# Kernel tuning notes

Measured on AMD Instinct MI355X. Metric: run time of the kernel, lower is better.

## Reference

```python
import jax, jax.numpy as jnp
import numpy as np

B, L, D, H = 2, 2048, 1024, 16
HD = D // H
ROPE_BASE = 10000.0


def _chain_info(lengths):
    """lengths: [B, L] int, chain lengths packed at the front, zeros after.
    Returns per-position within-chain positions (RoPE resets per chain),
    chain ids, and a validity mask."""
    def one(row):
        csum = jnp.cumsum(row)                      # [L]
        total = csum[-1]
        p = jnp.arange(L)
        cid = jnp.searchsorted(csum, p, side='right')  # chain id per position
        prev = jnp.where(cid > 0, csum[jnp.clip(cid - 1, 0, L - 1)], 0)
        valid = p < total
        pos = jnp.where(valid, p - prev, 0).astype(jnp.float32)
        return pos, cid, valid
    return jax.vmap(one)(lengths)


def _rope_tables(pos):
    # pos: [B, L] float -> cos/sin [B, L, 1, HD]
    inv_freq = 1.0 / (ROPE_BASE ** (jnp.arange(0, HD, 2, dtype=jnp.float32) / HD))
    freqs = pos[..., None] * inv_freq               # [B, L, HD/2]
    emb = jnp.concatenate([freqs, freqs], axis=-1)  # [B, L, HD]
    return jnp.cos(emb)[:, :, None, :], jnp.sin(emb)[:, :, None, :]


def _apply_rope(x, cos, sin):
    d = x.shape[-1]
    x1, x2 = x[..., : d // 2], x[..., d // 2:]
    return x * cos + jnp.concatenate([-x2, x1], axis=-1) * sin


def _branch(x, Wqkv, bqkv, cos, sin, allowed):
    # x: [B, L, D]; allowed: [B, L, L] bool attention mask for this branch
    qkv = x @ Wqkv.T + bqkv                          # [B, L, 3D]
    qkv = qkv.reshape(B, L, 3, H, HD)
    q, k, v = qkv[:, :, 0], qkv[:, :, 1], qkv[:, :, 2]
    q = q * (HD ** -0.5)
    q = _apply_rope(q, cos, sin)
    k = _apply_rope(k, cos, sin)
    scores = jnp.einsum('bthd,bshd->bhts', q, k)     # [B, H, L, L]
    scores = jnp.where(allowed[:, None], scores, -jnp.inf)
    probs = jax.nn.softmax(scores, axis=-1)
    probs = jnp.where(jnp.isnan(probs), 0.0, probs)  # fully-masked rows -> 0
    out = jnp.einsum('bhts,bshd->bthd', probs, v)    # [B, L, H, HD]
    return out.reshape(B, L, D)


def setup_inputs() -> dict:
    key = jax.random.key(0)
    ks = jax.random.split(key, 7)
    s = 0.02
    lens = np.zeros((B, L), np.int64)
    lens[0, :8] = [300, 250, 200, 400, 350, 248, 150, 100]   # sum 1998
    lens[1, :6] = [512, 400, 300, 360, 276, 200]             # sum 2048
    return {
        'hidden_states': jax.random.normal(ks[0], (B, L, D), jnp.float32),
        'attention_mask_in_length': jnp.asarray(lens),
        'Wqkv_intra': jax.random.normal(ks[1], (3 * D, D), jnp.float32) * s,
        'bqkv_intra': jnp.zeros((3 * D,), jnp.float32),
        'Wqkv_inter': jax.random.normal(ks[2], (3 * D, D), jnp.float32) * s,
        'bqkv_inter': jnp.zeros((3 * D,), jnp.float32),
        'Wout': jax.random.normal(ks[3], (D, D), jnp.float32) * s,
        'bout': jnp.zeros((D,), jnp.float32),
    }


def reference(hidden_states, attention_mask_in_length, Wqkv_intra, bqkv_intra,
              Wqkv_inter, bqkv_inter, Wout, bout):
    pos, cid, valid = _chain_info(attention_mask_in_length)
    cos, sin = _rope_tables(pos)
    same_chain = cid[:, :, None] == cid[:, None, :]          # [B, L, L]
    key_valid = valid[:, None, :]                            # [B, 1, L]
    allowed_intra = same_chain & key_valid
    allowed_inter = (~same_chain) & key_valid
    out_intra = _branch(hidden_states, Wqkv_intra, bqkv_intra, cos, sin, allowed_intra)
    out_inter = _branch(hidden_states, Wqkv_inter, bqkv_inter, cos, sin, allowed_inter)
    return (out_intra + out_inter) @ Wout.T + bout
```

## Files before the change

kernel.cpp:

```cpp
#include <hip/hip_runtime.h>
#include <hip/hip_bf16.h>
#include <stdint.h>

#define B 2
#define L 2048
#define D 1024
#define H 16
#define HD 64
#define NT (L / 64)
#define NQT (L / 128)
#define INVALID_CID 0x40000000
#define BHLHD ((size_t)B * H * L * HD)

typedef __hip_bfloat16 bf16;
typedef __attribute__((ext_vector_type(8))) short short8;
typedef __attribute__((ext_vector_type(4))) float floatx4;
typedef __attribute__((ext_vector_type(4))) unsigned int uint4v;

static __device__ __forceinline__ short f2bf(float f) {
    bf16 h = __float2bfloat16(f);
    return *reinterpret_cast<short*>(&h);
}

static __device__ __forceinline__ void async_copy16(const void* g, void* l) {
    __builtin_amdgcn_global_load_lds((__attribute__((address_space(1))) void*)g,
                                     (__attribute__((address_space(3))) void*)l,
                                     16, 0, 0);
}

__global__ void chain_kernel(const int* __restrict__ lens,
                             float* __restrict__ pos, int* __restrict__ cid,
                             int4* __restrict__ tinfo)
{
    __shared__ int csum[L];
    __shared__ int cids[L];
    __shared__ int part[256];
    int b = blockIdx.x;
    int t = threadIdx.x;

    int loc[8];
    int s = 0;
    #pragma unroll
    for (int j = 0; j < 8; ++j) { s += lens[b * L + t * 8 + j]; loc[j] = s; }
    part[t] = s;
    __syncthreads();
    if (t == 0) {
        int acc = 0;
        for (int i = 0; i < 256; ++i) { int v = part[i]; part[i] = acc; acc += v; }
    }
    __syncthreads();
    int base = part[t];
    #pragma unroll
    for (int j = 0; j < 8; ++j) csum[t * 8 + j] = base + loc[j];
    __syncthreads();

    int total = csum[L - 1];
    for (int p = t; p < L; p += 256) {
        int cv;
        if (p < total) {
            int lo = 0, hi = L;
            while (lo < hi) {
                int mid = (lo + hi) >> 1;
                if (csum[mid] <= p) lo = mid + 1; else hi = mid;
            }
            int prev = (lo > 0) ? csum[lo - 1] : 0;
            pos[b * L + p] = (float)(p - prev);
            cv = lo;
        } else {
            pos[b * L + p] = 0.f;
            cv = INVALID_CID;
        }
        cids[p] = cv;
        cid[b * L + p] = cv;
    }
    __syncthreads();
    if (t < NT) {
        int mn = 0x7fffffff, mx = -1, any = 0, all = 1;
        for (int j = 0; j < 64; ++j) {
            int cv = cids[t * 64 + j];
            if (cv != INVALID_CID) { any = 1; mn = min(mn, cv); mx = max(mx, cv); }
            else all = 0;
        }
        tinfo[b * NT + t] = make_int4(mn, mx, any | (all << 1), 0);
    }
}

__global__ void rope_table(const float* __restrict__ pos, float2* __restrict__ tab)
{
    int idx = blockIdx.x * 256 + threadIdx.x;
    int j = idx & 31, l = idx >> 5;
    float invf = exp2f(-(float)j * (13.287712379549449f / 32.f));
    float ang = pos[l] * invf;
    tab[idx] = make_float2(cosf(ang), sinf(ang));
}

__global__ void cast_all(const float* __restrict__ x,  const float* __restrict__ Wi,
                         const float* __restrict__ We, const float* __restrict__ Wo,
                         bf16* __restrict__ xb, bf16* __restrict__ Wib,
                         bf16* __restrict__ Web, bf16* __restrict__ Wob)
{
    int bid = blockIdx.x;
    const float* src; bf16* dst; int base;
    if      (bid < 4096)  { src = x;  dst = xb;  base = bid; }
    else if (bid < 7168)  { src = Wi; dst = Wib; base = bid - 4096; }
    else if (bid < 10240) { src = We; dst = Web; base = bid - 7168; }
    else                  { src = Wo; dst = Wob; base = bid - 10240; }
    int i = (base * 256 + threadIdx.x) * 4;
    float4 v = *(const float4*)(src + i);
    dst[i + 0] = __float2bfloat16(v.x);
    dst[i + 1] = __float2bfloat16(v.y);
    dst[i + 2] = __float2bfloat16(v.z);
    dst[i + 3] = __float2bfloat16(v.w);
}

__global__ __launch_bounds__(256, 4) void gemm_qkv(
    const bf16* __restrict__ A, const bf16* __restrict__ Bw,
    const float* __restrict__ bi, const float* __restrict__ be,
    const float2* __restrict__ tab,
    bf16* __restrict__ Qo, bf16* __restrict__ Ko, bf16* __restrict__ Vto)
{
    __shared__ short Smem[2 * 128 * 32];
    short* As = Smem;
    short* Bs = Smem + 128 * 32;

    int tid = threadIdx.x;
    int wave = tid >> 6, lane = tid & 63;
    int i15 = lane & 15, q8 = lane >> 4;
    int wm = wave & 1, wn = wave >> 1;
    int m0 = blockIdx.y * 128, n0 = blockIdx.x * 128;
    const int K = D;

    floatx4 acc[4][4];
    #pragma unroll
    for (int mt = 0; mt < 4; ++mt)
        #pragma unroll
        for (int nt = 0; nt < 4; ++nt) acc[mt][nt] = (floatx4){0.f, 0.f, 0.f, 0.f};

    const short* gA = (const short*)A  + (size_t)(m0 + wave * 32 + (lane >> 2)) * K + (lane & 3) * 8;
    const short* gB = (const short*)Bw + (size_t)(n0 + wave * 32 + (lane >> 2)) * K + (lane & 3) * 8;
    short* lA = As + wave * 1024;
    short* lB = Bs + wave * 1024;

    for (int kt = 0; kt < K; kt += 32) {
        __syncthreads();
        async_copy16(gA + kt,          lA);
        async_copy16(gA + 16 * K + kt, lA + 512);
        async_copy16(gB + kt,          lB);
        async_copy16(gB + 16 * K + kt, lB + 512);
        __syncthreads();

        short8 af[4], bfr[4];
        #pragma unroll
        for (int mt = 0; mt < 4; ++mt)
            af[mt] = *(const short8*)&As[(wm * 64 + mt * 16 + i15) * 32 + q8 * 8];
        #pragma unroll
        for (int nt = 0; nt < 4; ++nt)
            bfr[nt] = *(const short8*)&Bs[(wn * 64 + nt * 16 + i15) * 32 + q8 * 8];
        #pragma unroll
        for (int mt = 0; mt < 4; ++mt)
            #pragma unroll
            for (int nt = 0; nt < 4; ++nt)
                acc[mt][nt] = __builtin_amdgcn_mfma_f32_16x16x32_bf16(af[mt], bfr[nt], acc[mt][nt], 0, 0, 0);
    }

    int nb = n0 + wn * 64;
    int segw = nb >> 10;
    int br = (segw >= 3);
    int st = segw - 3 * br;
    int h = (nb >> 6) & (H - 1);
    int b = m0 >> 11;
    int lb = (m0 & (L - 1)) + wm * 64;

    float bv[4];
    #pragma unroll
    for (int nt = 0; nt < 4; ++nt) {
        int n = nb + nt * 16 + i15;
        bv[nt] = (n < 3 * D) ? bi[n] : be[n - 3 * D];
    }

    if (st != 2) {
        bf16* out = (st == 0 ? Qo : Ko) + (size_t)br * BHLHD;
        const size_t bh = (size_t)(b * H + h) * L;
        float qs = (st == 0) ? 0.18033688011111772f : 1.0f;
        #pragma unroll
        for (int mt = 0; mt < 4; ++mt) {
            #pragma unroll
            for (int rg = 0; rg < 4; ++rg) {
                int m = m0 + wm * 64 + mt * 16 + q8 * 4 + rg;
                int l = lb + mt * 16 + q8 * 4 + rg;
                float2 cs0 = tab[(size_t)m * 32 + i15];
                float2 cs1 = tab[(size_t)m * 32 + 16 + i15];
                size_t orow = (bh + l) * HD;
                #pragma unroll
                for (int nt = 0; nt < 4; ++nt) {
                    float x  = acc[mt][nt][rg] + bv[nt];
                    float pr = acc[mt][nt ^ 2][rg] + bv[nt ^ 2];
                    float cc = (nt & 1) ? cs1.x : cs0.x;
                    float ss = (nt & 1) ? cs1.y : cs0.y;
                    float v = qs * (x * cc + ((nt < 2) ? -pr : pr) * ss);
                    out[orow + nt * 16 + i15] = __float2bfloat16(v);
                }
            }
        }
    } else {
        bf16* out = Vto + (size_t)br * BHLHD;
        const size_t bhd = (size_t)(b * H + h) * HD;
        __syncthreads();
        short* vts = Smem + wave * 64 * 20;
        #pragma unroll
        for (int mt = 0; mt < 4; ++mt) {
            #pragma unroll
            for (int nt = 0; nt < 4; ++nt) {
                uint2 w;
                w.x = (unsigned)(unsigned short)f2bf(acc[mt][nt][0] + bv[nt]) |
                      ((unsigned)(unsigned short)f2bf(acc[mt][nt][1] + bv[nt]) << 16);
                w.y = (unsigned)(unsigned short)f2bf(acc[mt][nt][2] + bv[nt]) |
                      ((unsigned)(unsigned short)f2bf(acc[mt][nt][3] + bv[nt]) << 16);
                *(uint2*)&vts[(nt * 16 + i15) * 20 + q8 * 4] = w;
            }
            uint2 r0 = *(const uint2*)&vts[lane * 20 + 0];
            uint2 r1 = *(const uint2*)&vts[lane * 20 + 4];
            uint2 r2 = *(const uint2*)&vts[lane * 20 + 8];
            uint2 r3 = *(const uint2*)&vts[lane * 20 + 12];
            size_t ga = (bhd + lane) * L + lb + mt * 16;
            uint4v v0 = (uint4v){r0.x, r0.y, r1.x, r1.y};
            uint4v v1 = (uint4v){r2.x, r2.y, r3.x, r3.y};
            *(uint4v*)&out[ga]     = v0;
            *(uint4v*)&out[ga + 8] = v1;
        }
    }
}

__global__ __launch_bounds__(256, 4) void gemm128(
    const bf16* __restrict__ A, const bf16* __restrict__ Bw,
    const float* __restrict__ bias, void* __restrict__ Cout,
    int M, int N, int K, int c_bf16)
{
    __shared__ short As[128 * 32];
    __shared__ short Bs[128 * 32];

    int tid = threadIdx.x;
    int wave = tid >> 6, lane = tid & 63;
    int i15 = lane & 15, q8 = lane >> 4;
    int wm = wave & 1, wn = wave >> 1;
    int m0 = blockIdx.y * 128, n0 = blockIdx.x * 128;

    floatx4 acc[4][4];
    #pragma unroll
    for (int mt = 0; mt < 4; ++mt)
        #pragma unroll
        for (int nt = 0; nt < 4; ++nt) acc[mt][nt] = (floatx4){0.f, 0.f, 0.f, 0.f};

    const short* gA = (const short*)A  + (size_t)(m0 + wave * 32 + (lane >> 2)) * K + (lane & 3) * 8;
    const short* gB = (const short*)Bw + (size_t)(n0 + wave * 32 + (lane >> 2)) * K + (lane & 3) * 8;
    short* lA = As + wave * 1024;
    short* lB = Bs + wave * 1024;

    for (int kt = 0; kt < K; kt += 32) {
        __syncthreads();
        async_copy16(gA + kt,          lA);
        async_copy16(gA + 16 * K + kt, lA + 512);
        async_copy16(gB + kt,          lB);
        async_copy16(gB + 16 * K + kt, lB + 512);
        __syncthreads();

        short8 af[4], bfr[4];
        #pragma unroll
        for (int mt = 0; mt < 4; ++mt)
            af[mt] = *(const short8*)&As[(wm * 64 + mt * 16 + i15) * 32 + q8 * 8];
        #pragma unroll
        for (int nt = 0; nt < 4; ++nt)
            bfr[nt] = *(const short8*)&Bs[(wn * 64 + nt * 16 + i15) * 32 + q8 * 8];
        #pragma unroll
        for (int mt = 0; mt < 4; ++mt)
            #pragma unroll
            for (int nt = 0; nt < 4; ++nt)
                acc[mt][nt] = __builtin_amdgcn_mfma_f32_16x16x32_bf16(af[mt], bfr[nt], acc[mt][nt], 0, 0, 0);
    }

    #pragma unroll
    for (int nt = 0; nt < 4; ++nt) {
        int n = n0 + wn * 64 + nt * 16 + i15;
        float bv = bias[n];
        #pragma unroll
        for (int mt = 0; mt < 4; ++mt) {
            #pragma unroll
            for (int rg = 0; rg < 4; ++rg) {
                int m = m0 + wm * 64 + mt * 16 + q8 * 4 + rg;
                float v = acc[mt][nt][rg] + bv;
                if (c_bf16) ((bf16*)Cout)[(size_t)m * N + n] = __float2bfloat16(v);
                else        ((float*)Cout)[(size_t)m * N + n] = v;
            }
        }
    }
}

__global__ __launch_bounds__(256, 2) void attn7(
    const bf16* __restrict__ Qg, const bf16* __restrict__ Kgg, const bf16* __restrict__ Vtgg,
    const int* __restrict__ cid, const int4* __restrict__ tinfo,
    bf16* __restrict__ Out)
{
    __shared__ short Ks[2][64][72];
    __shared__ short Vs[2][64][72];
    __shared__ int cls0_s[NT], cls1_s[NT];
    __shared__ int list_s[2][NT];
    __shared__ int nlist_s[2];

    int tid = threadIdx.x;
    int wave = tid >> 6, lane = tid & 63;
    int i15 = lane & 15, q8 = lane >> 4;
    int workid = ((blockIdx.x & 7) << 6) | (blockIdx.x >> 3);
    int qt = workid & (NQT - 1);
    int h  = (workid >> 4) & (H - 1);
    int b  = workid >> 8;
    int q0 = qt * 128;
    const size_t bh  = (size_t)(b * H + h) * L;
    const size_t bhd = (size_t)(b * H + h) * HD;

    int cq[2];
    #pragma unroll
    for (int g = 0; g < 2; ++g)
        cq[g] = cid[b * L + q0 + g * 64 + wave * 16 + i15];

    int4 qa = tinfo[b * NT + 2 * qt];
    int4 qb4 = tinfo[b * NT + 2 * qt + 1];
    int4 qinf;
    qinf.x = min(qa.x, qb4.x);
    qinf.y = max(qa.y, qb4.y);
    qinf.z = ((qa.z | qb4.z) & 1) | (qa.z & qb4.z & 2);
    int qall = (qinf.z >> 1) & 1;

    if (tid < NT) {
        int4 ki = tinfo[b * NT + tid];
        int kany = ki.z & 1, kall = (ki.z >> 1) & 1;
        bool disjoint = (ki.x > qinf.y) || (ki.y < qinf.x);
        bool mono = qall && kall && (qinf.x == qinf.y) && (ki.x == ki.y) && (qinf.x == ki.x);
        cls0_s[tid] = (!kany || disjoint) ? 0 : (mono ? 2 : 1);
        cls1_s[tid] = (!kany || mono) ? 0 : ((kall && disjoint) ? 2 : 1);
    }
    __syncthreads();
    if (tid < 2) {
        const int* cls = tid ? cls1_s : cls0_s;
        int n = 0;
        for (int t = 0; t < NT; ++t) {
            int c = cls[t];
            if (c) list_s[tid][n++] = (t * 64) | ((c == 2) << 16);
        }
        nlist_s[tid] = n;
    }
    __syncthreads();

    int r = tid >> 2, ccol = (tid & 3) * 16;
    int sr = ((((r >> 2) & 1) | ((r >> 5) << 1)) << 4) | (((r >> 3) & 3) << 2) | (r & 3);

    floatx4 accO[2][2][4];
    #pragma unroll
    for (int br = 0; br < 2; ++br)
        #pragma unroll
        for (int g = 0; g < 2; ++g)
            #pragma unroll
            for (int t = 0; t < 4; ++t) accO[br][g][t] = (floatx4){0.f, 0.f, 0.f, 0.f};
    float lsum[2][2] = {{0.f, 0.f}, {0.f, 0.f}};

    #pragma unroll
    for (int br = 0; br < 2; ++br) {
        const short* Qb    = (const short*)Qg  + (size_t)br * BHLHD;
        const short* Kbase = (const short*)Kgg + (size_t)br * BHLHD + (bh + r) * HD + ccol;
        const short* Vbase = (const short*)Vtgg + (size_t)br * BHLHD + (bhd + r) * L + ccol;
        int n = nlist_s[br];

        short8 qf[2][2];
        #pragma unroll
        for (int g = 0; g < 2; ++g) {
            const short* qp = Qb + (bh + q0 + g * 64 + wave * 16 + i15) * HD + q8 * 8;
            qf[g][0] = *(const short8*)(qp);
            qf[g][1] = *(const short8*)(qp + 32);
        }

        int4 pk0, pk1, pv0, pv1;
        int cur = 0;
        if (n > 0) {
            cur = list_s[br][0];
            int kt0 = cur & 0xffff;
            pk0 = *(const int4*)(Kbase + (size_t)kt0 * HD);
            pk1 = *(const int4*)(Kbase + (size_t)kt0 * HD + 8);
            pv0 = *(const int4*)(Vbase + kt0);
            pv1 = *(const int4*)(Vbase + kt0 + 8);
        }
        __syncthreads();

        for (int i = 0; i < n; ++i) {
            int kt = cur & 0xffff, full = cur >> 16;
            int buf = i & 1;

            *(int4*)&Ks[buf][sr][ccol]     = pk0;
            *(int4*)&Ks[buf][sr][ccol + 8] = pk1;
            *(int4*)&Vs[buf][r][ccol]      = pv0;
            *(int4*)&Vs[buf][r][ccol + 8]  = pv1;
            __syncthreads();

            if (i + 1 < n) {
                cur = list_s[br][i + 1];
                int nk = cur & 0xffff;
                pk0 = *(const int4*)(Kbase + (size_t)nk * HD);
                pk1 = *(const int4*)(Kbase + (size_t)nk * HD + 8);
                pv0 = *(const int4*)(Vbase + nk);
                pv1 = *(const int4*)(Vbase + nk + 8);
            }

            unsigned int dl[2][4], dh[2][4];
            #pragma unroll
            for (int t = 0; t < 4; ++t) {
                short8 b0 = *(const short8*)&Ks[buf][t * 16 + i15][q8 * 8];
                short8 b1 = *(const short8*)&Ks[buf][t * 16 + i15][32 + q8 * 8];

                floatx4 accS[2];
                #pragma unroll
                for (int g = 0; g < 2; ++g) {
                    accS[g] = (floatx4){0.f, 0.f, 0.f, 0.f};
                    accS[g] = __builtin_amdgcn_mfma_f32_16x16x32_bf16(b0, qf[g][0], accS[g], 0, 0, 0);
                    accS[g] = __builtin_amdgcn_mfma_f32_16x16x32_bf16(b1, qf[g][1], accS[g], 0, 0, 0);
                }

                if (!full) {
                    int4 ck4 = *(const int4*)(cid + b * L + kt + (q8 << 3) + ((t & 1) << 2) + ((t >> 1) << 5));
                    int ckr[4] = {ck4.x, ck4.y, ck4.z, ck4.w};
                    #pragma unroll
                    for (int g = 0; g < 2; ++g)
                        #pragma unroll
                        for (int rg = 0; rg < 4; ++rg) {
                            bool kv = (ckr[rg] != INVALID_CID);
                            bool match = (cq[g] == ckr[rg]);
                            bool ok = kv && (br ? !match : match);
                            accS[g][rg] = ok ? accS[g][rg] : -1e30f;
                        }
                }

                #pragma unroll
                for (int g = 0; g < 2; ++g) {
                    float p0 = __builtin_amdgcn_exp2f(accS[g][0]);
                    float p1 = __builtin_amdgcn_exp2f(accS[g][1]);
                    float p2 = __builtin_amdgcn_exp2f(accS[g][2]);
                    float p3 = __builtin_amdgcn_exp2f(accS[g][3]);
                    lsum[br][g] += (p0 + p1) + (p2 + p3);
                    dl[g][t] = (unsigned)(unsigned short)f2bf(p0) | ((unsigned)(unsigned short)f2bf(p1) << 16);
                    dh[g][t] = (unsigned)(unsigned short)f2bf(p2) | ((unsigned)(unsigned short)f2bf(p3) << 16);
                }
            }

            union { uint4v u; short8 s; } pa0[2], pa1[2];
            #pragma unroll
            for (int g = 0; g < 2; ++g) {
                pa0[g].u = (uint4v){dl[g][0], dh[g][0], dl[g][1], dh[g][1]};
                pa1[g].u = (uint4v){dl[g][2], dh[g][2], dl[g][3], dh[g][3]};
            }

            #pragma unroll
            for (int dt = 0; dt < 4; ++dt) {
                short8 vf0 = *(const short8*)&Vs[buf][dt * 16 + i15][q8 * 8];
                short8 vf1 = *(const short8*)&Vs[buf][dt * 16 + i15][32 + q8 * 8];
                #pragma unroll
                for (int g = 0; g < 2; ++g) {
                    accO[br][g][dt] = __builtin_amdgcn_mfma_f32_16x16x32_bf16(pa0[g].s, vf0, accO[br][g][dt], 0, 0, 0);
                    accO[br][g][dt] = __builtin_amdgcn_mfma_f32_16x16x32_bf16(pa1[g].s, vf1, accO[br][g][dt], 0, 0, 0);
                }
            }
        }
    }

    float inv[2][2][4];
    #pragma unroll
    for (int br = 0; br < 2; ++br)
        #pragma unroll
        for (int g = 0; g < 2; ++g) {
            float ls = lsum[br][g];
            ls += __shfl_xor(ls, 16, 64);
            ls += __shfl_xor(ls, 32, 64);
            #pragma unroll
            for (int rg = 0; rg < 4; ++rg) {
                float lv = __shfl(ls, q8 * 4 + rg, 64);
                inv[br][g][rg] = (lv > 0.f) ? 1.f / lv : 0.f;
            }
        }

    #pragma unroll
    for (int g = 0; g < 2; ++g)
        #pragma unroll
        for (int t = 0; t < 4; ++t)
            #pragma unroll
            for (int rg = 0; rg < 4; ++rg) {
                size_t idx = (size_t)(b * L + q0 + g * 64 + wave * 16 + q8 * 4 + rg) * D + h * HD + t * 16 + i15;
                float o = accO[0][g][t][rg] * inv[0][g][rg] + accO[1][g][t][rg] * inv[1][g][rg];
                Out[idx] = __float2bfloat16(o);
            }
}

extern "C" void kernel_launch(void* const* d_in, const int* in_sizes, int n_in,
                              void* d_out, int out_size, void* d_ws, size_t ws_size,
                              hipStream_t stream)
{
    const float* x    = (const float*)d_in[0];
    const int*   mlen = (const int*)  d_in[1];
    const float* Wi   = (const float*)d_in[2];
    const float* bi   = (const float*)d_in[3];
    const float* We   = (const float*)d_in[4];
    const float* be   = (const float*)d_in[5];
    const float* Wo   = (const float*)d_in[6];
    const float* bo   = (const float*)d_in[7];

    char* ws = (char*)d_ws;
    size_t off = 0;
    auto alloc = [&](size_t bytes) {
        void* p = ws + off;
        off += (bytes + 255) & ~(size_t)255;
        return p;
    };
    bf16*  x_b   = (bf16*) alloc((size_t)B * L * D * 2);
    bf16*  Wi_b  = (bf16*) alloc((size_t)3 * D * D * 2);
    bf16*  We_b  = (bf16*) alloc((size_t)3 * D * D * 2);
    bf16*  Wo_b  = (bf16*) alloc((size_t)D * D * 2);
    bf16*  q_b   = (bf16*) alloc(2 * BHLHD * 2);
    bf16*  k_b   = (bf16*) alloc(2 * BHLHD * 2);
    bf16*  vt_b  = (bf16*) alloc(2 * BHLHD * 2);
    bf16*  sum_b = (bf16*) alloc((size_t)B * L * D * 2);
    float* pos   = (float*)alloc((size_t)B * L * 4);
    int*   cid   = (int*)  alloc((size_t)B * L * 4);
    int4*  tinfo = (int4*) alloc((size_t)B * NT * 16);
    float2* rtab = (float2*)alloc((size_t)B * L * 32 * 8);
    (void)ws_size; (void)n_in; (void)in_sizes; (void)out_size;

    chain_kernel<<<B, 256, 0, stream>>>(mlen, pos, cid, tinfo);
    rope_table<<<B * L * 32 / 256, 256, 0, stream>>>(pos, rtab);

    cast_all<<<11264, 256, 0, stream>>>(x, Wi, We, Wo, x_b, Wi_b, We_b, Wo_b);

    dim3 gq(6 * D / 128, B * L / 128);
    gemm_qkv<<<gq, 256, 0, stream>>>(x_b, Wi_b, bi, be, rtab, q_b, k_b, vt_b);

    attn7<<<B * H * NQT, 256, 0, stream>>>(q_b, k_b, vt_b, cid, tinfo, sum_b);

    dim3 go(D / 128, B * L / 128);
    gemm128<<<go, 256, 0, stream>>>(sum_b, Wo_b, bo, d_out, B * L, D, D, 0);
}
```

Baseline: 290.1 us.

## Double-buffer GEMM LDS tiles, fuse rope/cast prep, widen attention to 256-query blocks

Both GEMMs now double-buffer their LDS tiles, issuing the async global-to-LDS copy for the next K slice before computing the current one, which overlaps loads with MFMA work and removes one barrier per iteration. The rope table and cast kernels are merged into one launch to save launch overhead. The attention kernel now uses 512 threads covering 256 queries per block, so each K/V tile loaded into LDS is reused by twice as many queries and each thread loads half as much. The costs are double the LDS per GEMM block, which may lower occupancy, and half as many attention blocks.

```diff
diff --git a/kernel.cpp b/kernel.cpp
--- a/kernel.cpp
+++ b/kernel.cpp
@@ -8,7 +8,7 @@
 #define H 16
 #define HD 64
 #define NT (L / 64)
-#define NQT (L / 128)
+#define NQT2 (L / 256)
 #define INVALID_CID 0x40000000
 #define BHLHD ((size_t)B * H * L * HD)
 
@@ -85,32 +85,32 @@
     }
 }
 
-__global__ void rope_table(const float* __restrict__ pos, float2* __restrict__ tab)
-{
-    int idx = blockIdx.x * 256 + threadIdx.x;
-    int j = idx & 31, l = idx >> 5;
-    float invf = exp2f(-(float)j * (13.287712379549449f / 32.f));
-    float ang = pos[l] * invf;
-    tab[idx] = make_float2(cosf(ang), sinf(ang));
-}
-
-__global__ void cast_all(const float* __restrict__ x,  const float* __restrict__ Wi,
-                         const float* __restrict__ We, const float* __restrict__ Wo,
-                         bf16* __restrict__ xb, bf16* __restrict__ Wib,
-                         bf16* __restrict__ Web, bf16* __restrict__ Wob)
+__global__ void prep_kernel(const float* __restrict__ x,  const float* __restrict__ Wi,
+                            const float* __restrict__ We, const float* __restrict__ Wo,
+                            bf16* __restrict__ xb, bf16* __restrict__ Wib,
+                            bf16* __restrict__ Web, bf16* __restrict__ Wob,
+                            const float* __restrict__ pos, float2* __restrict__ tab)
 {
     int bid = blockIdx.x;
-    const float* src; bf16* dst; int base;
-    if      (bid < 4096)  { src = x;  dst = xb;  base = bid; }
-    else if (bid < 7168)  { src = Wi; dst = Wib; base = bid - 4096; }
-    else if (bid < 10240) { src = We; dst = Web; base = bid - 7168; }
-    else                  { src = Wo; dst = Wob; base = bid - 10240; }
-    int i = (base * 256 + threadIdx.x) * 4;
-    float4 v = *(const float4*)(src + i);
-    dst[i + 0] = __float2bfloat16(v.x);
-    dst[i + 1] = __float2bfloat16(v.y);
-    dst[i + 2] = __float2bfloat16(v.z);
-    dst[i + 3] = __float2bfloat16(v.w);
+    if (bid < 11264) {
+        const float* src; bf16* dst; int base;
+        if      (bid < 4096)  { src = x;  dst = xb;  base = bid; }
+        else if (bid < 7168)  { src = Wi; dst = Wib; base = bid - 4096; }
+        else if (bid < 10240) { src = We; dst = Web; base = bid - 7168; }
+        else                  { src = Wo; dst = Wob; base = bid - 10240; }
+        int i = (base * 256 + threadIdx.x) * 4;
+        float4 v = *(const float4*)(src + i);
+        dst[i + 0] = __float2bfloat16(v.x);
+        dst[i + 1] = __float2bfloat16(v.y);
+        dst[i + 2] = __float2bfloat16(v.z);
+        dst[i + 3] = __float2bfloat16(v.w);
+    } else {
+        int idx = (bid - 11264) * 256 + threadIdx.x;
+        int j = idx & 31, l = idx >> 5;
+        float invf = exp2f(-(float)j * (13.287712379549449f / 32.f));
+        float ang = pos[l] * invf;
+        tab[idx] = make_float2(cosf(ang), sinf(ang));
+    }
 }
 
 __global__ __launch_bounds__(256, 4) void gemm_qkv(
@@ -119,9 +119,7 @@
     const float2* __restrict__ tab,
     bf16* __restrict__ Qo, bf16* __restrict__ Ko, bf16* __restrict__ Vto)
 {
-    __shared__ short Smem[2 * 128 * 32];
-    short* As = Smem;
-    short* Bs = Smem + 128 * 32;
+    __shared__ short Smem[4 * 128 * 32];
 
     int tid = threadIdx.x;
     int wave = tid >> 6, lane = tid & 63;
@@ -138,17 +136,25 @@
 
     const short* gA = (const short*)A  + (size_t)(m0 + wave * 32 + (lane >> 2)) * K + (lane & 3) * 8;
     const short* gB = (const short*)Bw + (size_t)(n0 + wave * 32 + (lane >> 2)) * K + (lane & 3) * 8;
-    short* lA = As + wave * 1024;
-    short* lB = Bs + wave * 1024;
-
-    for (int kt = 0; kt < K; kt += 32) {
-        __syncthreads();
+
+    auto stage = [&](int bufp, int kt) {
+        short* lA = Smem + bufp * 8192 + wave * 1024;
+        short* lB = lA + 4096;
         async_copy16(gA + kt,          lA);
         async_copy16(gA + 16 * K + kt, lA + 512);
         async_copy16(gB + kt,          lB);
         async_copy16(gB + 16 * K + kt, lB + 512);
-        __syncthreads();
-
+    };
+
+    stage(0, 0);
+    __syncthreads();
+
+    int cur = 0;
+    for (int kt = 0; kt < K; kt += 32) {
+        if (kt + 32 < K) stage(cur ^ 1, kt + 32);
+
+        const short* As = Smem + cur * 8192;
+        const short* Bs = As + 4096;
         short8 af[4], bfr[4];
         #pragma unroll
         for (int mt = 0; mt < 4; ++mt)
@@ -161,6 +167,9 @@
             #pragma unroll
             for (int nt = 0; nt < 4; ++nt)
                 acc[mt][nt] = __builtin_amdgcn_mfma_f32_16x16x32_bf16(af[mt], bfr[nt], acc[mt][nt], 0, 0, 0);
+
+        __syncthreads();
+        cur ^= 1;
     }
 
     int nb = n0 + wn * 64;
@@ -236,8 +245,7 @@
     const float* __restrict__ bias, void* __restrict__ Cout,
     int M, int N, int K, int c_bf16)
 {
-    __shared__ short As[128 * 32];
-    __shared__ short Bs[128 * 32];
+    __shared__ short Smem[4 * 128 * 32];
 
     int tid = threadIdx.x;
     int wave = tid >> 6, lane = tid & 63;
@@ -253,17 +261,25 @@
 
     const short* gA = (const short*)A  + (size_t)(m0 + wave * 32 + (lane >> 2)) * K + (lane & 3) * 8;
     const short* gB = (const short*)Bw + (size_t)(n0 + wave * 32 + (lane >> 2)) * K + (lane & 3) * 8;
-    short* lA = As + wave * 1024;
-    short* lB = Bs + wave * 1024;
-
-    for (int kt = 0; kt < K; kt += 32) {
-        __syncthreads();
+
+    auto stage = [&](int bufp, int kt) {
+        short* lA = Smem + bufp * 8192 + wave * 1024;
+        short* lB = lA + 4096;
         async_copy16(gA + kt,          lA);
         async_copy16(gA + 16 * K + kt, lA + 512);
         async_copy16(gB + kt,          lB);
         async_copy16(gB + 16 * K + kt, lB + 512);
-        __syncthreads();
-
+    };
+
+    stage(0, 0);
+    __syncthreads();
+
+    int cur = 0;
+    for (int kt = 0; kt < K; kt += 32) {
+        if (kt + 32 < K) stage(cur ^ 1, kt + 32);
+
+        const short* As = Smem + cur * 8192;
+        const short* Bs = As + 4096;
         short8 af[4], bfr[4];
         #pragma unroll
         for (int mt = 0; mt < 4; ++mt)
@@ -276,6 +292,9 @@
             #pragma unroll
             for (int nt = 0; nt < 4; ++nt)
                 acc[mt][nt] = __builtin_amdgcn_mfma_f32_16x16x32_bf16(af[mt], bfr[nt], acc[mt][nt], 0, 0, 0);
+
+        __syncthreads();
+        cur ^= 1;
     }
 
     #pragma unroll
@@ -295,7 +314,7 @@
     }
 }
 
-__global__ __launch_bounds__(256, 2) void attn7(
+__global__ __launch_bounds__(512, 2) void attn11(
     const bf16* __restrict__ Qg, const bf16* __restrict__ Kgg, const bf16* __restrict__ Vtgg,
     const int* __restrict__ cid, const int4* __restrict__ tinfo,
     bf16* __restrict__ Out)
@@ -309,25 +328,29 @@
     int tid = threadIdx.x;
     int wave = tid >> 6, lane = tid & 63;
     int i15 = lane & 15, q8 = lane >> 4;
-    int workid = ((blockIdx.x & 7) << 6) | (blockIdx.x >> 3);
-    int qt = workid & (NQT - 1);
-    int h  = (workid >> 4) & (H - 1);
-    int b  = workid >> 8;
-    int q0 = qt * 128;
+    int workid = ((blockIdx.x & 7) << 5) | (blockIdx.x >> 3);
+    int qt = workid & (NQT2 - 1);
+    int h  = (workid >> 3) & (H - 1);
+    int b  = workid >> 7;
+    int q0 = qt * 256;
     const size_t bh  = (size_t)(b * H + h) * L;
     const size_t bhd = (size_t)(b * H + h) * HD;
 
     int cq[2];
     #pragma unroll
     for (int g = 0; g < 2; ++g)
-        cq[g] = cid[b * L + q0 + g * 64 + wave * 16 + i15];
-
-    int4 qa = tinfo[b * NT + 2 * qt];
-    int4 qb4 = tinfo[b * NT + 2 * qt + 1];
+        cq[g] = cid[b * L + q0 + g * 128 + wave * 16 + i15];
+
     int4 qinf;
-    qinf.x = min(qa.x, qb4.x);
-    qinf.y = max(qa.y, qb4.y);
-    qinf.z = ((qa.z | qb4.z) & 1) | (qa.z & qb4.z & 2);
+    {
+        int4 e0 = tinfo[b * NT + 4 * qt];
+        int4 e1 = tinfo[b * NT + 4 * qt + 1];
+        int4 e2 = tinfo[b * NT + 4 * qt + 2];
+        int4 e3 = tinfo[b * NT + 4 * qt + 3];
+        qinf.x = min(min(e0.x, e1.x), min(e2.x, e3.x));
+        qinf.y = max(max(e0.y, e1.y), max(e2.y, e3.y));
+        qinf.z = ((e0.z | e1.z | e2.z | e3.z) & 1) | (e0.z & e1.z & e2.z & e3.z & 2);
+    }
     int qall = (qinf.z >> 1) & 1;
 
     if (tid < NT) {
@@ -350,7 +373,7 @@
     }
     __syncthreads();
 
-    int r = tid >> 2, ccol = (tid & 3) * 16;
+    int r = tid >> 3, c8 = (tid & 7) * 8;
     int sr = ((((r >> 2) & 1) | ((r >> 5) << 1)) << 4) | (((r >> 3) & 3) << 2) | (r & 3);
 
     floatx4 accO[2][2][4];
@@ -364,28 +387,26 @@
 
     #pragma unroll
     for (int br = 0; br < 2; ++br) {
-        const short* Qb    = (const short*)Qg  + (size_t)br * BHLHD;
-        const short* Kbase = (const short*)Kgg + (size_t)br * BHLHD + (bh + r) * HD + ccol;
-        const short* Vbase = (const short*)Vtgg + (size_t)br * BHLHD + (bhd + r) * L + ccol;
+        const short* Qb    = (const short*)Qg   + (size_t)br * BHLHD;
+        const short* Kbase = (const short*)Kgg  + (size_t)br * BHLHD + (bh + r) * HD + c8;
+        const short* Vbase = (const short*)Vtgg + (size_t)br * BHLHD + (bhd + r) * L + c8;
         int n = nlist_s[br];
 
         short8 qf[2][2];
         #pragma unroll
         for (int g = 0; g < 2; ++g) {
-            const short* qp = Qb + (bh + q0 + g * 64 + wave * 16 + i15) * HD + q8 * 8;
+            const short* qp = Qb + (bh + q0 + g * 128 + wave * 16 + i15) * HD + q8 * 8;
             qf[g][0] = *(const short8*)(qp);
             qf[g][1] = *(const short8*)(qp + 32);
         }
 
-        int4 pk0, pk1, pv0, pv1;
+        int4 pk, pv;
         int cur = 0;
         if (n > 0) {
             cur = list_s[br][0];
             int kt0 = cur & 0xffff;
-            pk0 = *(const int4*)(Kbase + (size_t)kt0 * HD);
-            pk1 = *(const int4*)(Kbase + (size_t)kt0 * HD + 8);
-            pv0 = *(const int4*)(Vbase + kt0);
-            pv1 = *(const int4*)(Vbase + kt0 + 8);
+            pk = *(const int4*)(Kbase + (size_t)kt0 * HD);
+            pv = *(const int4*)(Vbase + kt0);
         }
         __syncthreads();
 
@@ -393,19 +414,15 @@
             int kt = cur & 0xffff, full = cur >> 16;
             int buf = i & 1;
 
-            *(int4*)&Ks[buf][sr][ccol]     = pk0;
-            *(int4*)&Ks[buf][sr][ccol + 8] = pk1;
-            *(int4*)&Vs[buf][r][ccol]      = pv0;
-            *(int4*)&Vs[buf][r][ccol + 8]  = pv1;
+            *(int4*)&Ks[buf][sr][c8] = pk;
+            *(int4*)&Vs[buf][r][c8]  = pv;
             __syncthreads();
 
             if (i + 1 < n) {
                 cur = list_s[br][i + 1];
                 int nk = cur & 0xffff;
-                pk0 = *(const int4*)(Kbase + (size_t)nk * HD);
-                pk1 = *(const int4*)(Kbase + (size_t)nk * HD + 8);
-                pv0 = *(const int4*)(Vbase + nk);
-                pv1 = *(const int4*)(Vbase + nk + 8);
+                pk = *(const int4*)(Kbase + (size_t)nk * HD);
+                pv = *(const int4*)(Vbase + nk);
             }
 
             unsigned int dl[2][4], dh[2][4];
@@ -489,7 +506,7 @@
         for (int t = 0; t < 4; ++t)
             #pragma unroll
             for (int rg = 0; rg < 4; ++rg) {
-                size_t idx = (size_t)(b * L + q0 + g * 64 + wave * 16 + q8 * 4 + rg) * D + h * HD + t * 16 + i15;
+                size_t idx = (size_t)(b * L + q0 + g * 128 + wave * 16 + q8 * 4 + rg) * D + h * HD + t * 16 + i15;
                 float o = accO[0][g][t][rg] * inv[0][g][rg] + accO[1][g][t][rg] * inv[1][g][rg];
                 Out[idx] = __float2bfloat16(o);
             }
@@ -530,14 +547,13 @@
     (void)ws_size; (void)n_in; (void)in_sizes; (void)out_size;
 
     chain_kernel<<<B, 256, 0, stream>>>(mlen, pos, cid, tinfo);
-    rope_table<<<B * L * 32 / 256, 256, 0, stream>>>(pos, rtab);
-
-    cast_all<<<11264, 256, 0, stream>>>(x, Wi, We, Wo, x_b, Wi_b, We_b, Wo_b);
+
+    prep_kernel<<<11776, 256, 0, stream>>>(x, Wi, We, Wo, x_b, Wi_b, We_b, Wo_b, pos, rtab);
 
     dim3 gq(6 * D / 128, B * L / 128);
     gemm_qkv<<<gq, 256, 0, stream>>>(x_b, Wi_b, bi, be, rtab, q_b, k_b, vt_b);
 
-    attn7<<<B * H * NQT, 256, 0, stream>>>(q_b, k_b, vt_b, cid, tinfo, sum_b);
+    attn11<<<B * H * NQT2, 512, 0, stream>>>(q_b, k_b, vt_b, cid, tinfo, sum_b);
 
     dim3 go(D / 128, B * L / 128);
     gemm128<<<go, 256, 0, stream>>>(sum_b, Wo_b, bo, d_out, B * L, D, D, 0);
```

Result: faster. 281.2 us (-3.1%).
